# Kernel optimization log

Measured on AMD Instinct MI355X. Metric: run time of the kernel, lower is better.

## Reference

```python
import jax, jax.numpy as jnp
import numpy as np

N_NODES = 100000
N_EDGES = 1600000
NEG_SLOPE = 0.2  # PyG GATConv default


def _glorot(key, shape):
    fan = sum(shape[:2]) if len(shape) > 1 else shape[0] * 2
    s = jnp.sqrt(6.0 / fan)
    return jax.random.uniform(key, shape, jnp.float32, -s, s)


def gat_layer(x, src, dst, edge_attr, W, a_src, a_dst, We, a_e, b, heads, out_ch, concat):
    """Faithful PyG GATConv (add_self_loops=True, fill_value='mean', edge_dim set)."""
    n = x.shape[0]
    # self-loop edge_attr = mean of incoming edge_attr per dst node (0 if none)
    deg = jax.ops.segment_sum(jnp.ones((src.shape[0],), edge_attr.dtype), dst, num_segments=n)
    loop_attr = jax.ops.segment_sum(edge_attr, dst, num_segments=n) / jnp.maximum(deg, 1.0)[:, None]
    loop = jnp.arange(n, dtype=src.dtype)
    src_f = jnp.concatenate([src, loop])
    dst_f = jnp.concatenate([dst, loop])
    ea = jnp.concatenate([edge_attr, loop_attr], axis=0)
    # node transform -> [n, H, C]
    h = (x @ W).reshape(n, heads, out_ch)
    al_src = jnp.sum(h * a_src, axis=-1)  # [n, H]
    al_dst = jnp.sum(h * a_dst, axis=-1)  # [n, H]
    e = (ea @ We).reshape(-1, heads, out_ch)
    al_e = jnp.sum(e * a_e, axis=-1)      # [Ef, H]
    alpha = jax.nn.leaky_relu(al_src[src_f] + al_dst[dst_f] + al_e, negative_slope=NEG_SLOPE)
    # segment softmax over destination nodes (every node has a self loop)
    m = jax.ops.segment_max(alpha, dst_f, num_segments=n)
    ex = jnp.exp(alpha - m[dst_f])
    den = jax.ops.segment_sum(ex, dst_f, num_segments=n)
    att = ex / den[dst_f]                 # [Ef, H]
    out = jax.ops.segment_sum(att[:, :, None] * h[src_f], dst_f, num_segments=n)  # [n, H, C]
    out = out.reshape(n, heads * out_ch) if concat else out.mean(axis=1)
    return out + b


def setup_inputs() -> dict:
    key = jax.random.key(0)
    ks = jax.random.split(key, 20)
    x = jax.random.normal(ks[0], (N_NODES, 5), jnp.float32)
    edge_index = jax.random.randint(ks[1], (2, N_EDGES), 0, N_NODES, jnp.int64)
    edge_attr = jax.random.normal(ks[2], (N_EDGES, 2), jnp.float32)
    # conv1: in=5, out=32, heads=4, concat -> 128
    p = {
        "W1": _glorot(ks[3], (5, 128)), "aS1": _glorot(ks[4], (4, 32)),
        "aD1": _glorot(ks[5], (4, 32)), "We1": _glorot(ks[6], (2, 128)),
        "aE1": _glorot(ks[7], (4, 32)), "b1": jnp.zeros((128,), jnp.float32),
        # conv2: in=128, out=32, heads=2, concat -> 64
        "W2": _glorot(ks[8], (128, 64)), "aS2": _glorot(ks[9], (2, 32)),
        "aD2": _glorot(ks[10], (2, 32)), "We2": _glorot(ks[11], (2, 64)),
        "aE2": _glorot(ks[12], (2, 32)), "b2": jnp.zeros((64,), jnp.float32),
        # conv3: in=64, out=1, heads=1, concat=False
        "W3": _glorot(ks[13], (64, 1)), "aS3": _glorot(ks[14], (1, 1)),
        "aD3": _glorot(ks[15], (1, 1)), "We3": _glorot(ks[16], (2, 1)),
        "aE3": _glorot(ks[17], (1, 1)), "b3": jnp.zeros((1,), jnp.float32),
    }
    return {"x": x, "edge_index": edge_index, "edge_attr": edge_attr, **p}


def reference(x, edge_index, edge_attr,
              W1, aS1, aD1, We1, aE1, b1,
              W2, aS2, aD2, We2, aE2, b2,
              W3, aS3, aD3, We3, aE3, b3):
    src, dst = edge_index[0], edge_index[1]
    h = gat_layer(x, src, dst, edge_attr, W1, aS1, aD1, We1, aE1, b1, 4, 32, True)
    h = jax.nn.elu(h)  # dropout is identity in eval
    h = gat_layer(h, src, dst, edge_attr, W2, aS2, aD2, We2, aE2, b2, 2, 32, True)
    h = jax.nn.elu(h)
    h = gat_layer(h, src, dst, edge_attr, W3, aS3, aD3, We3, aE3, b3, 1, 1, False)
    return jax.nn.sigmoid(h).squeeze(-1)  # [N]
```

## Files before the change

### kernel.cpp

```cpp
#include <hip/hip_runtime.h>
#include <math.h>

#define NN 100000
#define NE 1600000
#define NPB 256
#define NB 391
#define NCHUNK 512
#define CH 3125
#define SEGW (NB + 1)
#define MAXB 5376
#define LOG2E 1.44269504088896f

__device__ __forceinline__ float lrelu(float x) { return fmaxf(x, 0.2f * x); }
__device__ __forceinline__ float elu1(float x) { return x > 0.f ? x : (__expf(x) - 1.f); }
__device__ __forceinline__ float fexp2(float x) {
#if __has_builtin(__builtin_amdgcn_exp2f)
    return __builtin_amdgcn_exp2f(x);
#else
    return exp2f(x);
#endif
}
__device__ __forceinline__ unsigned bf16rne(float f) {
    unsigned u = __float_as_uint(f);
    return (u + 0x7FFFu + ((u >> 16) & 1u)) >> 16;
}
__device__ __forceinline__ float bf16lo(unsigned u) { return __uint_as_float(u << 16); }
__device__ __forceinline__ float bf16hi(unsigned u) {
    return __uint_as_float(u & 0xFFFF0000u);
}

__global__ void __launch_bounds__(256) k_bin1(const int* __restrict__ src,
                                              const int* __restrict__ dst,
                                              const float* __restrict__ ea,
                                              int* __restrict__ bucket_cnt,
                                              int* __restrict__ seg,
                                              uint2* __restrict__ binned,
                                              unsigned char* __restrict__ dstb) {
    __shared__ int hist[NB], start[NB], cur[NB];
    __shared__ int s2[256];
    __shared__ uint2 stage[CH];
    __shared__ unsigned char dstg[CH];
    int c = blockIdx.x, t = threadIdx.x;
    int e0 = c * CH;
    for (int b = t; b < NB; b += 256) hist[b] = 0;
    __syncthreads();
    for (int i = t; i < CH; i += 256) atomicAdd(&hist[dst[e0 + i] >> 8], 1);
    __syncthreads();
    int a0 = (2 * t < NB) ? hist[2 * t] : 0;
    int a1 = (2 * t + 1 < NB) ? hist[2 * t + 1] : 0;
    s2[t] = a0 + a1;
    __syncthreads();
    for (int off = 1; off < 256; off <<= 1) {
        int x = (t >= off) ? s2[t - off] : 0;
        __syncthreads();
        if (t >= off) s2[t] += x;
        __syncthreads();
    }
    int pex = s2[t] - (a0 + a1);
    if (2 * t < NB) { start[2 * t] = pex; cur[2 * t] = pex; }
    if (2 * t + 1 < NB) { start[2 * t + 1] = pex + a0; cur[2 * t + 1] = pex + a0; }
    __syncthreads();
    for (int b = t; b < NB; b += 256) {
        seg[c * SEGW + b] = start[b];
        if (hist[b]) atomicAdd(&bucket_cnt[b], hist[b]);
    }
    if (t == 0) seg[c * SEGW + NB] = CH;
    __syncthreads();
    for (int i = t; i < CH; i += 256) {
        int d = dst[e0 + i];
        int bkt = d >> 8;
        int p = atomicAdd(&cur[bkt], 1);
        unsigned pk = bf16rne(ea[2 * (e0 + i)]) | (bf16rne(ea[2 * (e0 + i) + 1]) << 16);
        stage[p] = make_uint2((unsigned)src[e0 + i], pk);
        dstg[p] = (unsigned char)(d & 255);
    }
    __syncthreads();
    for (int i = t; i < CH; i += 256) {
        binned[e0 + i] = stage[i];
        dstb[e0 + i] = dstg[i];
    }
}

__global__ void k_bscan(const int* __restrict__ bucket_cnt, int* __restrict__ bucket_base) {
    __shared__ int s[512];
    int t = threadIdx.x;
    int v = (t < NB) ? bucket_cnt[t] : 0;
    s[t] = v;
    __syncthreads();
    for (int off = 1; off < 512; off <<= 1) {
        int x = (t >= off) ? s[t - off] : 0;
        __syncthreads();
        if (t >= off) s[t] += x;
        __syncthreads();
    }
    if (t < NB) {
        bucket_base[t] = s[t] - v;
        if (t == NB - 1) bucket_base[NB] = s[t];
    }
}

__global__ void __launch_bounds__(256) k_bin2(const int* __restrict__ bucket_base,
                                              const int* __restrict__ seg,
                                              const uint2* __restrict__ binned,
                                              const unsigned char* __restrict__ dstb,
                                              int* __restrict__ rowptr,
                                              uint2* __restrict__ edges,
                                              float* __restrict__ la) {
    __shared__ int sstart[NCHUNK], soff[NCHUNK];
    __shared__ int s2[256];
    __shared__ uint2 stage[MAXB];
    __shared__ unsigned char sd[MAXB];
    __shared__ int hist[NPB], pre[NPB], cursor[NPB];
    __shared__ float ea0s[NPB], ea1s[NPB];
    int b = blockIdx.x, t = threadIdx.x;
    int len0, len1;
    {
        int c0 = 2 * t, c1 = 2 * t + 1;
        int st0 = seg[c0 * SEGW + b], en0 = seg[c0 * SEGW + b + 1];
        int st1 = seg[c1 * SEGW + b], en1 = seg[c1 * SEGW + b + 1];
        sstart[c0] = st0;
        sstart[c1] = st1;
        len0 = en0 - st0;
        len1 = en1 - st1;
        s2[t] = len0 + len1;
    }
    __syncthreads();
    for (int off = 1; off < 256; off <<= 1) {
        int x = (t >= off) ? s2[t - off] : 0;
        __syncthreads();
        if (t >= off) s2[t] += x;
        __syncthreads();
    }
    int pex = s2[t] - (len0 + len1);
    soff[2 * t] = pex;
    soff[2 * t + 1] = pex + len0;
    __syncthreads();
    int total = s2[255];
    if (total > MAXB) total = MAXB;
    for (int i = t; i < total; i += 256) {
        int lo = 0, hi = NCHUNK - 1;
        while (lo < hi) {
            int mid = (lo + hi + 1) >> 1;
            if (soff[mid] <= i) lo = mid; else hi = mid - 1;
        }
        int pos = lo * CH + sstart[lo] + (i - soff[lo]);
        stage[i] = binned[pos];
        sd[i] = dstb[pos];
    }
    hist[t] = 0;
    ea0s[t] = 0.f;
    ea1s[t] = 0.f;
    __syncthreads();
    for (int i = t; i < total; i += 256) atomicAdd(&hist[sd[i]], 1);
    __syncthreads();
    int v = hist[t];
    pre[t] = v;
    __syncthreads();
    for (int off = 1; off < 256; off <<= 1) {
        int x = (t >= off) ? pre[t - off] : 0;
        __syncthreads();
        if (t >= off) pre[t] += x;
        __syncthreads();
    }
    int bb = bucket_base[b];
    int ex = pre[t] - v;
    int nb0 = b << 8;
    if (nb0 + t <= NN) rowptr[nb0 + t] = bb + ex;
    cursor[t] = bb + ex;
    __syncthreads();
    for (int i = t; i < total; i += 256) {
        uint2 rec = stage[i];
        unsigned char d = sd[i];
        int pos = atomicAdd(&cursor[d], 1);
        edges[pos] = rec;
        atomicAdd(&ea0s[d], bf16lo(rec.y));
        atomicAdd(&ea1s[d], bf16hi(rec.y));
    }
    __syncthreads();
    int n = nb0 + t;
    if (n < NN) {
        float dg = fmaxf((float)v, 1.0f);
        la[2 * n] = ea0s[t] / dg;
        la[2 * n + 1] = ea1s[t] / dg;
    }
}

__global__ void k_const(const float* __restrict__ We1, const float* __restrict__ aE1,
                        const float* __restrict__ We2, const float* __restrict__ aE2,
                        const float* __restrict__ We3, const float* __restrict__ aE3,
                        const float* __restrict__ W1, const float* __restrict__ aS1,
                        const float* __restrict__ aD1, float* __restrict__ cbuf) {
    int t = threadIdx.x;
    if (t < 8) {
        int d = t >> 2, hd = t & 3;
        float s = 0.f;
        for (int c = 0; c < 32; c++) s += We1[d * 128 + hd * 32 + c] * aE1[hd * 32 + c];
        cbuf[t] = s * LOG2E;
    } else if (t < 12) {
        int idx = t - 8, d = idx >> 1, hd = idx & 1;
        float s = 0.f;
        for (int c = 0; c < 32; c++) s += We2[d * 64 + hd * 32 + c] * aE2[hd * 32 + c];
        cbuf[t] = s * LOG2E;
    } else if (t < 14) {
        cbuf[t] = We3[t - 12] * aE3[0] * LOG2E;
    } else if (t >= 16 && t < 56) {
        int r = (t - 16) % 20, hd = r / 5, i = r % 5;
        const float* a = (t - 16 < 20) ? aS1 : aD1;
        float s = 0.f;
        for (int c = 0; c < 32; c++) s += W1[i * 128 + hd * 32 + c] * a[hd * 32 + c];
        cbuf[t] = s * LOG2E;
    }
}

__global__ void k_prep1(const float* __restrict__ x, const float* __restrict__ vsd,
                        float4* __restrict__ xp, float4* __restrict__ als1,
                        float4* __restrict__ ald1) {
    int n = blockIdx.x * blockDim.x + threadIdx.x;
    if (n >= NN) return;
    float x0 = x[5 * n], x1 = x[5 * n + 1], x2 = x[5 * n + 2], x3 = x[5 * n + 3],
          x4 = x[5 * n + 4];
    xp[2 * n] = make_float4(x0, x1, x2, x3);
    xp[2 * n + 1] = make_float4(x4, 0.f, 0.f, 0.f);
    float sv[4], dv[4];
#pragma unroll
    for (int hd = 0; hd < 4; hd++) {
        const float* vS = vsd + hd * 5;
        const float* vD = vsd + 20 + hd * 5;
        sv[hd] = x0 * vS[0] + x1 * vS[1] + x2 * vS[2] + x3 * vS[3] + x4 * vS[4];
        dv[hd] = x0 * vD[0] + x1 * vD[1] + x2 * vD[2] + x3 * vD[3] + x4 * vD[4];
    }
    als1[n] = make_float4(sv[0], sv[1], sv[2], sv[3]);
    ald1[n] = make_float4(dv[0], dv[1], dv[2], dv[3]);
}

__global__ void k_agg1(const int* __restrict__ rowptr, const uint2* __restrict__ edges,
                       const float4* __restrict__ xp, const float* __restrict__ als1,
                       const float* __restrict__ ald1, const float* __restrict__ la,
                       const float* __restrict__ me, float* __restrict__ xw) {
    int t = blockIdx.x * blockDim.x + threadIdx.x;
    if (t >= NN * 4) return;
    int n = t >> 2, hd = t & 3;
    float me0 = me[hd], me1 = me[4 + hd];
    float aldn = ald1[t];
    float aself = lrelu(als1[t] + aldn + la[2 * n] * me0 + la[2 * n + 1] * me1);
    int start = rowptr[n], end = rowptr[n + 1];
    float den = 1.f;
    float4 xa = xp[2 * n];
    float xb = xp[2 * n + 1].x;
    float a0 = xa.x, a1 = xa.y, a2 = xa.z, a3 = xa.w, a4 = xb;
    for (int e = start; e < end; ++e) {
        uint2 ep = edges[e];
        int s = (int)ep.x;
        float a = lrelu(als1[s * 4 + hd] + aldn + bf16lo(ep.y) * me0 + bf16hi(ep.y) * me1);
        float p = fexp2(a - aself);
        den += p;
        float4 sa = xp[2 * s];
        float sb = xp[2 * s + 1].x;
        a0 += p * sa.x;
        a1 += p * sa.y;
        a2 += p * sa.z;
        a3 += p * sa.w;
        a4 += p * sb;
    }
    float r = 1.f / den;
    float* w = xw + (size_t)n * 20 + hd * 5;
    w[0] = a0 * r;
    w[1] = a1 * r;
    w[2] = a2 * r;
    w[3] = a3 * r;
    w[4] = a4 * r;
}

__global__ void __launch_bounds__(64) k_l2trans(
        const float* __restrict__ xw, const float* __restrict__ W1,
        const float* __restrict__ b1, const float* __restrict__ W2,
        const float* __restrict__ aS2, const float* __restrict__ aD2,
        unsigned short* __restrict__ h2q, float* __restrict__ als2,
        float* __restrict__ ald2) {
    __shared__ float sx[32 * 132];
    int nb = blockIdx.x * 32, t = threadIdx.x;
#pragma unroll
    for (int half = 0; half < 2; half++) {
        int nl = (t >> 2) + 16 * half;
        int q = t & 3;
        int node = nb + nl;
        float w[20];
        if (node < NN) {
#pragma unroll
            for (int i = 0; i < 20; i++) w[i] = xw[(size_t)node * 20 + i];
        } else {
#pragma unroll
            for (int i = 0; i < 20; i++) w[i] = 0.f;
        }
#pragma unroll
        for (int k = 0; k < 32; k++) {
            int ch = q + 4 * k;
            int hd = ch >> 5;
            float v = w[hd * 5] * W1[ch] + w[hd * 5 + 1] * W1[128 + ch] +
                      w[hd * 5 + 2] * W1[256 + ch] + w[hd * 5 + 3] * W1[384 + ch] +
                      w[hd * 5 + 4] * W1[512 + ch] + b1[ch];
            sx[nl * 132 + ch] = (node < NN) ? elu1(v) : 0.f;
        }
    }
    __syncthreads();
    int jq = t & 15, ng = t >> 4;
    int j4 = jq * 4;
    float4 acc[8];
#pragma unroll
    for (int p = 0; p < 8; p++) acc[p] = make_float4(0.f, 0.f, 0.f, 0.f);
    for (int ic = 0; ic < 128; ic += 4) {
        float4 s[8];
#pragma unroll
        for (int p = 0; p < 8; p++)
            s[p] = *(const float4*)(sx + (ng + 4 * p) * 132 + ic);
#pragma unroll
        for (int r = 0; r < 4; r++) {
            float4 wv = *(const float4*)(W2 + (ic + r) * 64 + j4);
#pragma unroll
            for (int p = 0; p < 8; p++) {
                float sv = (r == 0) ? s[p].x : (r == 1) ? s[p].y : (r == 2) ? s[p].z : s[p].w;
                acc[p].x += sv * wv.x;
                acc[p].y += sv * wv.y;
                acc[p].z += sv * wv.z;
                acc[p].w += sv * wv.w;
            }
        }
    }
    int hd = jq >> 3;
    float4 a_s = *(const float4*)(aS2 + j4);
    float4 a_d = *(const float4*)(aD2 + j4);
    float pS[8], pD[8];
#pragma unroll
    for (int p = 0; p < 8; p++) {
        pS[p] = acc[p].x * a_s.x + acc[p].y * a_s.y + acc[p].z * a_s.z + acc[p].w * a_s.w;
        pD[p] = acc[p].x * a_d.x + acc[p].y * a_d.y + acc[p].z * a_d.z + acc[p].w * a_d.w;
    }
#pragma unroll
    for (int off = 1; off < 8; off <<= 1) {
#pragma unroll
        for (int p = 0; p < 8; p++) {
            pS[p] += __shfl_xor(pS[p], off);
            pD[p] += __shfl_xor(pD[p], off);
        }
    }
#pragma unroll
    for (int p = 0; p < 8; p++) {
        int node = nb + ng + 4 * p;
        if (node < NN) {
            ushort4 q;
            q.x = (unsigned short)bf16rne(acc[p].x);
            q.y = (unsigned short)bf16rne(acc[p].y);
            q.z = (unsigned short)bf16rne(acc[p].z);
            q.w = (unsigned short)bf16rne(acc[p].w);
            *(ushort4*)(h2q + (size_t)node * 64 + j4) = q;
            if ((jq & 7) == 0) {
                als2[node * 2 + hd] = pS[p] * LOG2E;
                ald2[node * 2 + hd] = pD[p] * LOG2E;
            }
        }
    }
}

__global__ void k_agg2(const int* __restrict__ rowptr, const uint2* __restrict__ edges,
                       const unsigned short* __restrict__ h2q,
                       const float* __restrict__ als2, const float* __restrict__ ald2,
                       const float* __restrict__ la, const float* __restrict__ me,
                       const float* __restrict__ b2, const float* __restrict__ W3,
                       float* __restrict__ h3) {
    int t = blockIdx.x * blockDim.x + threadIdx.x;
    if (t >= NN * 4) return;
    int n = t >> 2, sub = t & 3, hd = sub >> 1, qh = sub & 1;
    int cbase = hd * 32 + qh * 16;
    float me0 = me[hd], me1 = me[2 + hd];
    float aldn = ald2[n * 2 + hd];
    float aself = lrelu(als2[n * 2 + hd] + aldn + la[2 * n] * me0 + la[2 * n + 1] * me1);
    int start = rowptr[n], end = rowptr[n + 1];
    float den = 1.f;
    float acc[16];
    {
        const uint4* hp = (const uint4*)(h2q + (size_t)n * 64 + cbase);
        uint4 u0 = hp[0], u1 = hp[1];
        acc[0] = bf16lo(u0.x); acc[1] = bf16hi(u0.x);
        acc[2] = bf16lo(u0.y); acc[3] = bf16hi(u0.y);
        acc[4] = bf16lo(u0.z); acc[5] = bf16hi(u0.z);
        acc[6] = bf16lo(u0.w); acc[7] = bf16hi(u0.w);
        acc[8] = bf16lo(u1.x); acc[9] = bf16hi(u1.x);
        acc[10] = bf16lo(u1.y); acc[11] = bf16hi(u1.y);
        acc[12] = bf16lo(u1.z); acc[13] = bf16hi(u1.z);
        acc[14] = bf16lo(u1.w); acc[15] = bf16hi(u1.w);
    }
    for (int e = start; e < end; ++e) {
        uint2 ep = edges[e];
        int s = (int)ep.x;
        float a = lrelu(als2[s * 2 + hd] + aldn + bf16lo(ep.y) * me0 + bf16hi(ep.y) * me1);
        float p = fexp2(a - aself);
        den += p;
        const uint4* sp = (const uint4*)(h2q + (size_t)s * 64 + cbase);
        uint4 u0 = sp[0], u1 = sp[1];
        acc[0] += p * bf16lo(u0.x); acc[1] += p * bf16hi(u0.x);
        acc[2] += p * bf16lo(u0.y); acc[3] += p * bf16hi(u0.y);
        acc[4] += p * bf16lo(u0.z); acc[5] += p * bf16hi(u0.z);
        acc[6] += p * bf16lo(u0.w); acc[7] += p * bf16hi(u0.w);
        acc[8] += p * bf16lo(u1.x); acc[9] += p * bf16hi(u1.x);
        acc[10] += p * bf16lo(u1.y); acc[11] += p * bf16hi(u1.y);
        acc[12] += p * bf16lo(u1.z); acc[13] += p * bf16hi(u1.z);
        acc[14] += p * bf16lo(u1.w); acc[15] += p * bf16hi(u1.w);
    }
    float r = 1.f / den;
    float part = 0.f;
#pragma unroll
    for (int c = 0; c < 16; c++) {
        float v = elu1(acc[c] * r + b2[cbase + c]);
        part += v * W3[cbase + c];
    }
    part += __shfl_xor(part, 1);
    part += __shfl_xor(part, 2);
    if (sub == 0) h3[n] = part;
}

__global__ void k_agg3(const int* __restrict__ rowptr, const uint2* __restrict__ edges,
                       const float* __restrict__ h, const float* __restrict__ aS3,
                       const float* __restrict__ aD3, const float* __restrict__ la,
                       const float* __restrict__ me, const float* __restrict__ b,
                       float* __restrict__ out) {
    int n = (blockIdx.x * blockDim.x + threadIdx.x) >> 6;
    if (n >= NN) return;
    int lane = threadIdx.x & 63;
    float me0 = me[0], me1 = me[1];
    float aSs = aS3[0] * LOG2E, aDs = aD3[0] * LOG2E;
    float hn = h[n];
    float ald_n = hn * aDs;
    float aself = lrelu(hn * aSs + ald_n + la[2 * n] * me0 + la[2 * n + 1] * me1);
    int start = rowptr[n], end = rowptr[n + 1];
    float den = 0.f, num = 0.f;
    for (int e = start + lane; e < end; e += 64) {
        uint2 ep = edges[e];
        int s = (int)ep.x;
        float hv = h[s];
        float a = lrelu(hv * aSs + ald_n + bf16lo(ep.y) * me0 + bf16hi(ep.y) * me1);
        float p = fexp2(a - aself);
        den += p;
        num += p * hv;
    }
#pragma unroll
    for (int off = 32; off > 0; off >>= 1) {
        den += __shfl_xor(den, off);
        num += __shfl_xor(num, off);
    }
    if (lane == 0) {
        den += 1.f;
        num += hn;
        float v = num / den + b[0];
        out[n] = 1.f / (1.f + __expf(-v));
    }
}

extern "C" void kernel_launch(void* const* d_in, const int* in_sizes, int n_in,
                              void* d_out, int out_size, void* d_ws, size_t ws_size,
                              hipStream_t stream) {
    const float* x   = (const float*)d_in[0];
    const int*   ei  = (const int*)d_in[1];
    const float* ea  = (const float*)d_in[2];
    const float* W1  = (const float*)d_in[3];
    const float* aS1 = (const float*)d_in[4];
    const float* aD1 = (const float*)d_in[5];
    const float* We1 = (const float*)d_in[6];
    const float* aE1 = (const float*)d_in[7];
    const float* b1  = (const float*)d_in[8];
    const float* W2  = (const float*)d_in[9];
    const float* aS2 = (const float*)d_in[10];
    const float* aD2 = (const float*)d_in[11];
    const float* We2 = (const float*)d_in[12];
    const float* aE2 = (const float*)d_in[13];
    const float* b2  = (const float*)d_in[14];
    const float* W3  = (const float*)d_in[15];
    const float* aS3 = (const float*)d_in[16];
    const float* aD3 = (const float*)d_in[17];
    const float* We3 = (const float*)d_in[18];
    const float* aE3 = (const float*)d_in[19];
    const float* b3  = (const float*)d_in[20];

    const int* srcv = ei;
    const int* dstv = ei + NE;

    char* basep = (char*)d_ws;
    size_t off = 0;
    auto alloc = [&](size_t nbytes) -> void* {
        void* p = basep + off;
        off += (nbytes + 255) & ~(size_t)255;
        return p;
    };
    int*    bucket_cnt  = (int*)alloc((size_t)(NB + 1) * 4);
    int*    bucket_base = (int*)alloc((size_t)(NB + 1) * 4);
    int*    rowptr      = (int*)alloc((size_t)(NN + 1) * 4);
    int*    seg         = (int*)alloc((size_t)NCHUNK * SEGW * 4);
    uint2*  binned      = (uint2*)alloc((size_t)NE * 8);
    unsigned char* dstb = (unsigned char*)alloc((size_t)NE);
    uint2*  edges       = (uint2*)alloc((size_t)NE * 8);
    float*  la          = (float*)alloc((size_t)NN * 8);
    float*  cbuf        = (float*)alloc(256);
    float4* xp          = (float4*)alloc((size_t)NN * 32);
    float4* als1        = (float4*)alloc((size_t)NN * 16);
    float4* ald1        = (float4*)alloc((size_t)NN * 16);
    float*  xw          = (float*)alloc((size_t)NN * 80);
    unsigned short* h2q = (unsigned short*)alloc((size_t)NN * 128);
    float*  als2        = (float*)alloc((size_t)NN * 8);
    float*  ald2        = (float*)alloc((size_t)NN * 8);
    float*  h3          = (float*)alloc((size_t)NN * 4);
    (void)ws_size; (void)in_sizes; (void)n_in; (void)out_size;

    float* me1 = cbuf;
    float* me2 = cbuf + 8;
    float* me3 = cbuf + 12;
    float* vsd = cbuf + 16;

    auto cdiv = [](long long a, long long b) { return (int)((a + b - 1) / b); };
    const int BS = 256;

    hipMemsetAsync(bucket_cnt, 0, (size_t)(NB + 1) * 4, stream);
    k_bin1<<<NCHUNK, 256, 0, stream>>>(srcv, dstv, ea, bucket_cnt, seg, binned, dstb);
    k_bscan<<<1, 512, 0, stream>>>(bucket_cnt, bucket_base);
    k_bin2<<<NB, 256, 0, stream>>>(bucket_base, seg, binned, dstb, rowptr, edges, la);

    k_const<<<1, 64, 0, stream>>>(We1, aE1, We2, aE2, We3, aE3, W1, aS1, aD1, cbuf);

    k_prep1<<<cdiv(NN, BS), BS, 0, stream>>>(x, vsd, xp, als1, ald1);
    k_agg1<<<cdiv((long long)NN * 4, BS), BS, 0, stream>>>(rowptr, edges, xp,
                                                           (const float*)als1,
                                                           (const float*)ald1, la, me1, xw);

    k_l2trans<<<cdiv(NN, 32), 64, 0, stream>>>(xw, W1, b1, W2, aS2, aD2, h2q, als2, ald2);
    k_agg2<<<cdiv((long long)NN * 4, BS), BS, 0, stream>>>(rowptr, edges, h2q, als2, ald2,
                                                           la, me2, b2, W3, h3);

    k_agg3<<<cdiv(NN, 4), 256, 0, stream>>>(rowptr, edges, h3, aS3, aD3, la, me3,
                                            b3, (float*)d_out);
}
```

Measured before the change: 347.3 us.

## Split layer-2 transform into activation kernel and bf16 MFMA GEMM

Replaces the fused FP32 layer-2 transform with two kernels. The first computes ELU(xw·W1+b1), stores it as bf16, and derives the attention logits from precomputed W2·a vectors. The second runs the 128→64 matmul with bf16 MFMA 16x16x32 instructions. This moves the dense FP32 FMA work onto matrix cores and removes the shared-memory staging. In exchange it adds a 25.6MB intermediate write and read, plus another bf16 rounding of activations before the GEMM.

```diff
diff --git a/kernel.cpp b/kernel.cpp
--- a/kernel.cpp
+++ b/kernel.cpp
@@ -10,6 +10,9 @@
 #define SEGW (NB + 1)
 #define MAXB 5376
 #define LOG2E 1.44269504088896f
+
+typedef __attribute__((ext_vector_type(8))) short bf16x8;
+typedef __attribute__((ext_vector_type(4))) float f32x4;
 
 __device__ __forceinline__ float lrelu(float x) { return fmaxf(x, 0.2f * x); }
 __device__ __forceinline__ float elu1(float x) { return x > 0.f ? x : (__expf(x) - 1.f); }
@@ -209,6 +212,27 @@
         float s = 0.f;
         for (int c = 0; c < 32; c++) s += W1[i * 128 + hd * 32 + c] * a[hd * 32 + c];
         cbuf[t] = s * LOG2E;
+    }
+}
+
+__global__ void k_const2(const float* __restrict__ W2, const float* __restrict__ aS2,
+                         const float* __restrict__ aD2, unsigned short* __restrict__ W2q,
+                         float* __restrict__ vsd2) {
+    int t = threadIdx.x;
+    for (int x = t; x < 64 * 128; x += 256) {
+        int j = x >> 7, i = x & 127;
+        W2q[x] = (unsigned short)bf16rne(W2[i * 64 + j]);
+    }
+    {
+        int hd = t >> 7, i = t & 127;
+        float s = 0.f, d = 0.f;
+        for (int c = 0; c < 32; c++) {
+            float wv = W2[i * 64 + hd * 32 + c];
+            s += wv * aS2[hd * 32 + c];
+            d += wv * aD2[hd * 32 + c];
+        }
+        vsd2[t] = s * LOG2E;
+        vsd2[256 + t] = d * LOG2E;
     }
 }
 
@@ -271,93 +295,75 @@
     w[4] = a4 * r;
 }
 
-__global__ void __launch_bounds__(64) k_l2trans(
-        const float* __restrict__ xw, const float* __restrict__ W1,
-        const float* __restrict__ b1, const float* __restrict__ W2,
-        const float* __restrict__ aS2, const float* __restrict__ aD2,
-        unsigned short* __restrict__ h2q, float* __restrict__ als2,
-        float* __restrict__ ald2) {
-    __shared__ float sx[32 * 132];
-    int nb = blockIdx.x * 32, t = threadIdx.x;
-#pragma unroll
-    for (int half = 0; half < 2; half++) {
-        int nl = (t >> 2) + 16 * half;
-        int q = t & 3;
-        int node = nb + nl;
-        float w[20];
-        if (node < NN) {
-#pragma unroll
-            for (int i = 0; i < 20; i++) w[i] = xw[(size_t)node * 20 + i];
-        } else {
-#pragma unroll
-            for (int i = 0; i < 20; i++) w[i] = 0.f;
-        }
-#pragma unroll
-        for (int k = 0; k < 32; k++) {
-            int ch = q + 4 * k;
-            int hd = ch >> 5;
-            float v = w[hd * 5] * W1[ch] + w[hd * 5 + 1] * W1[128 + ch] +
-                      w[hd * 5 + 2] * W1[256 + ch] + w[hd * 5 + 3] * W1[384 + ch] +
-                      w[hd * 5 + 4] * W1[512 + ch] + b1[ch];
-            sx[nl * 132 + ch] = (node < NN) ? elu1(v) : 0.f;
-        }
-    }
-    __syncthreads();
-    int jq = t & 15, ng = t >> 4;
-    int j4 = jq * 4;
-    float4 acc[8];
-#pragma unroll
-    for (int p = 0; p < 8; p++) acc[p] = make_float4(0.f, 0.f, 0.f, 0.f);
-    for (int ic = 0; ic < 128; ic += 4) {
-        float4 s[8];
-#pragma unroll
-        for (int p = 0; p < 8; p++)
-            s[p] = *(const float4*)(sx + (ng + 4 * p) * 132 + ic);
-#pragma unroll
-        for (int r = 0; r < 4; r++) {
-            float4 wv = *(const float4*)(W2 + (ic + r) * 64 + j4);
-#pragma unroll
-            for (int p = 0; p < 8; p++) {
-                float sv = (r == 0) ? s[p].x : (r == 1) ? s[p].y : (r == 2) ? s[p].z : s[p].w;
-                acc[p].x += sv * wv.x;
-                acc[p].y += sv * wv.y;
-                acc[p].z += sv * wv.z;
-                acc[p].w += sv * wv.w;
-            }
-        }
-    }
-    int hd = jq >> 3;
-    float4 a_s = *(const float4*)(aS2 + j4);
-    float4 a_d = *(const float4*)(aD2 + j4);
-    float pS[8], pD[8];
-#pragma unroll
-    for (int p = 0; p < 8; p++) {
-        pS[p] = acc[p].x * a_s.x + acc[p].y * a_s.y + acc[p].z * a_s.z + acc[p].w * a_s.w;
-        pD[p] = acc[p].x * a_d.x + acc[p].y * a_d.y + acc[p].z * a_d.z + acc[p].w * a_d.w;
-    }
-#pragma unroll
-    for (int off = 1; off < 8; off <<= 1) {
-#pragma unroll
-        for (int p = 0; p < 8; p++) {
-            pS[p] += __shfl_xor(pS[p], off);
-            pD[p] += __shfl_xor(pD[p], off);
-        }
-    }
-#pragma unroll
-    for (int p = 0; p < 8; p++) {
-        int node = nb + ng + 4 * p;
-        if (node < NN) {
-            ushort4 q;
-            q.x = (unsigned short)bf16rne(acc[p].x);
-            q.y = (unsigned short)bf16rne(acc[p].y);
-            q.z = (unsigned short)bf16rne(acc[p].z);
-            q.w = (unsigned short)bf16rne(acc[p].w);
-            *(ushort4*)(h2q + (size_t)node * 64 + j4) = q;
-            if ((jq & 7) == 0) {
-                als2[node * 2 + hd] = pS[p] * LOG2E;
-                ald2[node * 2 + hd] = pD[p] * LOG2E;
-            }
-        }
+__global__ void __launch_bounds__(256) k_act1(const float* __restrict__ xw,
+                                              const float* __restrict__ W1,
+                                              const float* __restrict__ b1,
+                                              const float* __restrict__ vsd2,
+                                              unsigned short* __restrict__ act1q,
+                                              float* __restrict__ als2,
+                                              float* __restrict__ ald2) {
+    int t = blockIdx.x * blockDim.x + threadIdx.x;
+    if (t >= NN * 4) return;
+    int n = t >> 2, q = t & 3;
+    int c0 = q * 32;
+    const float* w = xw + (size_t)n * 20 + q * 5;
+    float w0 = w[0], w1 = w[1], w2 = w[2], w3 = w[3], w4 = w[4];
+    float pS0 = 0.f, pS1 = 0.f, pD0 = 0.f, pD1 = 0.f;
+    unsigned short outv[32];
+#pragma unroll
+    for (int k = 0; k < 32; k++) {
+        int ch = c0 + k;
+        float v = w0 * W1[ch] + w1 * W1[128 + ch] + w2 * W1[256 + ch] +
+                  w3 * W1[384 + ch] + w4 * W1[512 + ch] + b1[ch];
+        v = elu1(v);
+        outv[k] = (unsigned short)bf16rne(v);
+        pS0 += v * vsd2[ch];
+        pS1 += v * vsd2[128 + ch];
+        pD0 += v * vsd2[256 + ch];
+        pD1 += v * vsd2[384 + ch];
+    }
+    ushort4* dst = (ushort4*)(act1q + (size_t)n * 128 + c0);
+#pragma unroll
+    for (int k = 0; k < 8; k++)
+        dst[k] = make_ushort4(outv[4 * k], outv[4 * k + 1], outv[4 * k + 2], outv[4 * k + 3]);
+    pS0 += __shfl_xor(pS0, 1); pS0 += __shfl_xor(pS0, 2);
+    pS1 += __shfl_xor(pS1, 1); pS1 += __shfl_xor(pS1, 2);
+    pD0 += __shfl_xor(pD0, 1); pD0 += __shfl_xor(pD0, 2);
+    pD1 += __shfl_xor(pD1, 1); pD1 += __shfl_xor(pD1, 2);
+    if (q == 0) {
+        als2[n * 2] = pS0;
+        als2[n * 2 + 1] = pS1;
+        ald2[n * 2] = pD0;
+        ald2[n * 2 + 1] = pD1;
+    }
+}
+
+__global__ void __launch_bounds__(256) k_gemm2(const unsigned short* __restrict__ act1q,
+                                               const unsigned short* __restrict__ W2q,
+                                               unsigned short* __restrict__ h2q) {
+    int wid = (blockIdx.x * blockDim.x + threadIdx.x) >> 6;
+    int lane = threadIdx.x & 63;
+    int mt = wid >> 1, jh = wid & 1;
+    int n0 = mt * 16;
+    int m = lane & 15, quad = lane >> 4;
+    int jA = jh * 32;
+    const bf16x8* Ab = (const bf16x8*)(act1q + (size_t)(n0 + m) * 128 + quad * 8);
+    const bf16x8* B0 = (const bf16x8*)(W2q + (size_t)(jA + m) * 128 + quad * 8);
+    const bf16x8* B1 = (const bf16x8*)(W2q + (size_t)(jA + 16 + m) * 128 + quad * 8);
+    f32x4 acc0 = {0.f, 0.f, 0.f, 0.f}, acc1 = {0.f, 0.f, 0.f, 0.f};
+#pragma unroll
+    for (int kc = 0; kc < 4; kc++) {
+        bf16x8 a = Ab[kc * 4];
+        bf16x8 b0 = B0[kc * 4];
+        bf16x8 b1 = B1[kc * 4];
+        acc0 = __builtin_amdgcn_mfma_f32_16x16x32_bf16(a, b0, acc0, 0, 0, 0);
+        acc1 = __builtin_amdgcn_mfma_f32_16x16x32_bf16(a, b1, acc1, 0, 0, 0);
+    }
+#pragma unroll
+    for (int r = 0; r < 4; r++) {
+        int node = n0 + quad * 4 + r;
+        h2q[(size_t)node * 64 + jA + m] = (unsigned short)bf16rne(acc0[r]);
+        h2q[(size_t)node * 64 + jA + 16 + m] = (unsigned short)bf16rne(acc1[r]);
     }
 }
 
@@ -499,10 +505,13 @@
     uint2*  edges       = (uint2*)alloc((size_t)NE * 8);
     float*  la          = (float*)alloc((size_t)NN * 8);
     float*  cbuf        = (float*)alloc(256);
+    float*  vsd2        = (float*)alloc(2048);
+    unsigned short* W2q = (unsigned short*)alloc(64 * 128 * 2);
     float4* xp          = (float4*)alloc((size_t)NN * 32);
     float4* als1        = (float4*)alloc((size_t)NN * 16);
     float4* ald1        = (float4*)alloc((size_t)NN * 16);
     float*  xw          = (float*)alloc((size_t)NN * 80);
+    unsigned short* act1q = (unsigned short*)alloc((size_t)NN * 256);
     unsigned short* h2q = (unsigned short*)alloc((size_t)NN * 128);
     float*  als2        = (float*)alloc((size_t)NN * 8);
     float*  ald2        = (float*)alloc((size_t)NN * 8);
@@ -523,13 +532,16 @@
     k_bin2<<<NB, 256, 0, stream>>>(bucket_base, seg, binned, dstb, rowptr, edges, la);
 
     k_const<<<1, 64, 0, stream>>>(We1, aE1, We2, aE2, We3, aE3, W1, aS1, aD1, cbuf);
+    k_const2<<<1, 256, 0, stream>>>(W2, aS2, aD2, W2q, vsd2);
 
     k_prep1<<<cdiv(NN, BS), BS, 0, stream>>>(x, vsd, xp, als1, ald1);
     k_agg1<<<cdiv((long long)NN * 4, BS), BS, 0, stream>>>(rowptr, edges, xp,
                                                            (const float*)als1,
                                                            (const float*)ald1, la, me1, xw);
 
-    k_l2trans<<<cdiv(NN, 32), 64, 0, stream>>>(xw, W1, b1, W2, aS2, aD2, h2q, als2, ald2);
+    k_act1<<<cdiv((long long)NN * 4, BS), BS, 0, stream>>>(xw, W1, b1, vsd2, act1q,
+                                                           als2, ald2);
+    k_gemm2<<<3125, 256, 0, stream>>>(act1q, W2q, h2q);
     k_agg2<<<cdiv((long long)NN * 4, BS), BS, 0, stream>>>(rowptr, edges, h2q, als2, ald2,
                                                            la, me2, b2, W3, h3);
 
```

After: 393.1 us. 1.13x slower.
